# Kernel optimization log

Measured on AMD Instinct MI355X. Metric: run time of the kernel, lower is better.

## Reference

```python
import jax, jax.numpy as jnp
import numpy as np
from jax import lax

B, C, H, W = 8, 512, 48, 48
E = 512          # embed_dim (== in_channels, required by GLoR fusion channel math)
P = 128          # ContextBlock planes = int(512*0.25)
NC = 2           # num_classes; also used (buggily, but faithfully) as BGAM threshold
TOPK_RATIO = 0.1


def conv1x1(x, w, b=None):
    # w: [out, in]
    y = jnp.einsum('bchw,oc->bohw', x, w)
    if b is not None:
        y = y + b[None, :, None, None]
    return y


def conv3x3(x, w, b):
    y = lax.conv_general_dilated(x, w, (1, 1), 'SAME',
                                 dimension_numbers=('NCHW', 'OIHW', 'NCHW'))
    return y + b[None, :, None, None]


def dwconv3x3(x, w):
    # depthwise: w [C,1,3,3], feature_group_count=C
    return lax.conv_general_dilated(x, w, (1, 1), 'SAME',
                                    dimension_numbers=('NCHW', 'OIHW', 'NCHW'),
                                    feature_group_count=x.shape[1])


def bn_eval(x, g, b):
    # eval-mode BatchNorm2d, running_mean=0, running_var=1, eps=1e-5
    scale = g / jnp.sqrt(1.0 + 1e-5)
    return x * scale[None, :, None, None] + b[None, :, None, None]


def chan_mlp(c, w1, b1, g, bl, w2, b2):
    # ContextBlock channel transform: 1x1 conv -> LayerNorm([P,1,1]) -> ReLU -> 1x1 conv, on [B,C] vectors
    h = c @ w1.T + b1                                  # [B,P]
    mu = h.mean(-1, keepdims=True)
    var = jnp.var(h, axis=-1, keepdims=True)
    h = (h - mu) / jnp.sqrt(var + 1e-5) * g + bl
    h = jax.nn.relu(h)
    return h @ w2.T + b2                               # [B,C]


def cos_self(t):
    # torch F.cosine_similarity(t, t, dim=1): dot/(max(n,eps)*max(n,eps)), eps=1e-8
    nrm2 = jnp.sum(t * t, axis=1)                      # [B,H,W]
    n = jnp.maximum(jnp.sqrt(nrm2), 1e-8)
    return nrm2 / (n * n)


def setup_inputs() -> dict:
    key = jax.random.key(0)
    ks = iter(jax.random.split(key, 64))
    def nrm(shape, scale):
        return (jax.random.normal(next(ks), shape) * scale).astype(jnp.float32)
    def gma(n):
        return (1.0 + 0.05 * jax.random.normal(next(ks), (n,))).astype(jnp.float32)
    def bta(n):
        return (0.05 * jax.random.normal(next(ks), (n,))).astype(jnp.float32)
    sC = 1.0 / np.sqrt(C)
    return dict(
        x=jax.random.normal(next(ks), (B, C, H, W), jnp.float32),
        # GLoR local ConvBranch
        lb_w1=nrm((E, C), sC), lb_g1=gma(E), lb_b1=bta(E),
        lb_w2=nrm((E, 1, 3, 3), 1.0 / 3.0), lb_g2=gma(E), lb_b2=bta(E),
        lb_w3=nrm((E, E), 1.0 / np.sqrt(E)), lb_g3=gma(E), lb_b3=bta(E),
        # GLoR ContextBlock (att pooling, channel_add + channel_mul)
        cm_w=nrm((1, C), sC), cm_b=bta(1),
        ca_w1=nrm((P, C), sC), ca_b1=bta(P), ca_lg=gma(P), ca_lb=bta(P),
        ca_w2=nrm((C, P), 1.0 / np.sqrt(P)), ca_b2=bta(C),
        cmu_w1=nrm((P, C), sC), cmu_b1=bta(P), cmu_lg=gma(P), cmu_lb=bta(P),
        cmu_w2=nrm((C, P), 1.0 / np.sqrt(P)), cmu_b2=bta(C),
        fu_w=nrm((E, 2 * E), 1.0 / np.sqrt(2 * E)), fu_b=bta(E),
        # heads
        sh_w=nrm((NC, E), 1.0 / np.sqrt(E)), sh_b=bta(NC),
        bh_w=nrm((2, E), 1.0 / np.sqrt(E)), bh_b=bta(2),
        # ReverseAttention
        ra_w1=nrm((2, 2, 3, 3), 1.0 / np.sqrt(18)), ra_b1=bta(2), ra_g1=gma(2), ra_bb1=bta(2),
        ra_w2=nrm((2, 2, 3, 3), 1.0 / np.sqrt(18)), ra_b2=bta(2), ra_g2=gma(2), ra_bb2=bta(2),
        # AGCR (all bias=False)
        q_w=nrm((E // 4, E), 1.0 / np.sqrt(E)), k_w=nrm((E // 4, E), 1.0 / np.sqrt(E)),
        v_w=nrm((E, E), 1.0 / np.sqrt(E)), fin_w=nrm((E, 2 * E), 1.0 / np.sqrt(2 * E)),
    )


def reference(x, lb_w1, lb_g1, lb_b1, lb_w2, lb_g2, lb_b2, lb_w3, lb_g3, lb_b3,
              cm_w, cm_b, ca_w1, ca_b1, ca_lg, ca_lb, ca_w2, ca_b2,
              cmu_w1, cmu_b1, cmu_lg, cmu_lb, cmu_w2, cmu_b2, fu_w, fu_b,
              sh_w, sh_b, bh_w, bh_b,
              ra_w1, ra_b1, ra_g1, ra_bb1, ra_w2, ra_b2, ra_g2, ra_bb2,
              q_w, k_w, v_w, fin_w):
    b_, c_, h_, w_ = x.shape
    N = h_ * w_
    # ---- GLoR: local ConvBranch ----
    t = jax.nn.relu(bn_eval(conv1x1(x, lb_w1), lb_g1, lb_b1))
    t = jax.nn.relu(bn_eval(dwconv3x3(t, lb_w2), lb_g2, lb_b2))
    local = bn_eval(conv1x1(t, lb_w3), lb_g3, lb_b3)
    # ---- GLoR: ContextBlock (att pooling) ----
    xf = x.reshape(b_, c_, N)
    mask = (conv1x1(x, cm_w, cm_b)).reshape(b_, 1, N)
    mask = jax.nn.softmax(mask, axis=2)
    ctx = jnp.einsum('bcn,bn->bc', xf, mask[:, 0, :])              # [B,C]
    mul = jax.nn.sigmoid(chan_mlp(ctx, cmu_w1, cmu_b1, cmu_lg, cmu_lb, cmu_w2, cmu_b2))
    add = chan_mlp(ctx, ca_w1, ca_b1, ca_lg, ca_lb, ca_w2, ca_b2)
    glob = x * mul[:, :, None, None] + add[:, :, None, None]
    gx = conv1x1(jnp.concatenate([local, glob], axis=1), fu_w, fu_b)  # [B,E,H,W]
    # ---- heads ----
    sem = conv1x1(gx, sh_w, sh_b)                                   # [B,NC,H,W]
    bdl = conv1x1(gx, bh_w, bh_b)                                   # [B,2,H,W]
    # ---- ReverseAttention(boundary_logits, sigmoid(boundary_logits)) ----
    wx = bdl * (1.0 - jax.nn.sigmoid(bdl))
    r = jax.nn.relu(bn_eval(conv3x3(wx, ra_w1, ra_b1), ra_g1, ra_bb1))
    r = jax.nn.relu(bn_eval(conv3x3(r, ra_w2, ra_b2), ra_g2, ra_bb2))
    # ---- BGAM (threshold = num_classes, faithful to source) ----
    thr = jnp.float32(NC)
    st = (cos_self(sem) > thr).astype(x.dtype)
    bt = (cos_self(r) > thr).astype(x.dtype)
    region = ((1.0 - st) * (1.0 - bt))[:, None]                     # [B,1,H,W]
    # ---- AGCR custom attention ----
    k_num = int(N * TOPK_RATIO)
    q = conv1x1(gx, q_w).reshape(b_, -1, N)                         # [B,E/4,N]
    kk = conv1x1(gx, k_w).reshape(b_, -1, N)
    v = conv1x1(gx, v_w).reshape(b_, E, N)
    attn = jnp.einsum('bdm,bdn->bmn', q, kk) / jnp.sqrt(jnp.float32(q.shape[1]))
    aw = jax.nn.softmax(attn, axis=-1)                              # [B,N,N]
    topv, _ = lax.top_k(aw, k_num)
    soft = topv.mean(-1)                                            # [B,N]
    aw = aw * soft[:, None, :]
    # bmm(value, aw^T).mean(-1) == value @ aw.mean(rows)
    col_mean = aw.mean(axis=1)                                      # [B,N]
    ctx2 = jnp.einsum('bcn,bn->bc', v, col_mean)                    # [B,E]
    ctx2 = jnp.broadcast_to(ctx2[:, :, None, None], gx.shape)
    refined = jnp.concatenate([gx, ctx2 * region], axis=1)          # [B,2E,H,W]
    return conv1x1(refined, fin_w)                                  # [B,E,H,W]
```

## Files before the change

### kernel.cpp

```cpp
#include <hip/hip_runtime.h>
#include <math.h>

#define NPIX 2304
#define NCH  512
#define NB   8
#define KNUM 230

typedef unsigned short u16;
typedef __attribute__((ext_vector_type(8))) short short8v;
typedef __attribute__((ext_vector_type(4))) float float4v;

__device__ __forceinline__ float bf2f(u16 u) {
    union { unsigned v; float f; } x; x.v = ((unsigned)u) << 16; return x.f;
}
__device__ __forceinline__ u16 f2bf(float f) {
    union { float f; unsigned v; } x; x.f = f;
    unsigned r = x.v + 0x7FFFu + ((x.v >> 16) & 1u);
    return (u16)(r >> 16);
}

__device__ __forceinline__ float waveSum(float v) {
    #pragma unroll
    for (int o = 32; o > 0; o >>= 1) v += __shfl_down(v, o);
    return v;
}
__device__ __forceinline__ float blockSum256(float v, float* sc4) {
    v = waveSum(v);
    __syncthreads();
    if ((threadIdx.x & 63) == 0) sc4[threadIdx.x >> 6] = v;
    __syncthreads();
    return sc4[0] + sc4[1] + sc4[2] + sc4[3];
}
__device__ __forceinline__ float waveMaxF(float v) {
    #pragma unroll
    for (int o = 32; o > 0; o >>= 1) v = fmaxf(v, __shfl_down(v, o));
    return v;
}
__device__ __forceinline__ float blockMax256(float v, float* sc4) {
    v = waveMaxF(v);
    __syncthreads();
    if ((threadIdx.x & 63) == 0) sc4[threadIdx.x >> 6] = v;
    __syncthreads();
    return fmaxf(fmaxf(sc4[0], sc4[1]), fmaxf(sc4[2], sc4[3]));
}

__device__ __forceinline__ void gl_lds16(const u16* g, u16* l) {
    __builtin_amdgcn_global_load_lds(
        reinterpret_cast<const unsigned __attribute__((address_space(1)))*>(
            reinterpret_cast<uintptr_t>(g)),
        reinterpret_cast<unsigned __attribute__((address_space(3)))*>(
            reinterpret_cast<uintptr_t>(l)),
        16, 0, 0);
}

__global__ __launch_bounds__(256, 2) void mfma_gemm(
    const u16* __restrict__ A, int ldA, long sA,
    const u16* __restrict__ B0, const u16* __restrict__ B1, int ldB, long sB,
    void* __restrict__ outp, int ldO, long sO,
    const float* __restrict__ scaleR, const float* __restrict__ biasR,
    const float* __restrict__ biasC, int ldbc,
    int K, float alpha, int flags)
{
    __shared__ u16 lA[128 * 64];
    __shared__ u16 lB[128 * 64];
    const int t  = threadIdx.x;
    const int w  = t >> 6, l = t & 63;
    const int wR = w >> 1, wC = w & 1;
    const int lg = l >> 4, lr = l & 15, l7 = l & 7;
    const int b   = blockIdx.z;
    const int Cl0 = blockIdx.x * 128;
    const int R0  = blockIdx.y * 128;
    const u16* Ab  = A + (size_t)b * sA;
    const u16* B0b = B0 + (size_t)b * sB;
    const u16* B1b = B1 ? B1 + (size_t)b * sB : nullptr;

    float4v acc[4][4];
    const float4v zero = {0.f, 0.f, 0.f, 0.f};
    #pragma unroll
    for (int i = 0; i < 4; ++i)
        #pragma unroll
        for (int j = 0; j < 4; ++j) acc[i][j] = zero;

    const int sr = t >> 3;
    const int sp = t & 7;

    for (int k0 = 0; k0 < K; k0 += 64) {
        const u16* Bsrc = B0b; int kb = k0;
        if (B1b && k0 >= 512) { Bsrc = B1b; kb = k0 - 512; }
        #pragma unroll
        for (int i = 0; i < 4; ++i) {
            const int r  = i * 32 + sr;
            const int ca = sp ^ (r & 7);
            gl_lds16(Ab   + (size_t)(R0  + r) * ldA + (k0 + ca * 8), &lA[i * 2048 + t * 8]);
            gl_lds16(Bsrc + (size_t)(Cl0 + r) * ldB + (kb + ca * 8), &lB[i * 2048 + t * 8]);
        }
        __syncthreads();
        #pragma unroll
        for (int kk = 0; kk < 2; ++kk) {
            short8v af[4], bfv[4];
            const int p = (kk * 4 + lg) ^ l7;
            #pragma unroll
            for (int mt = 0; mt < 4; ++mt) {
                const int rA = wR * 64 + mt * 16 + lr;
                af[mt]  = *reinterpret_cast<const short8v*>(&lA[rA * 64 + p * 8]);
                const int rB = wC * 64 + mt * 16 + lr;
                bfv[mt] = *reinterpret_cast<const short8v*>(&lB[rB * 64 + p * 8]);
            }
            #pragma unroll
            for (int mt = 0; mt < 4; ++mt)
                #pragma unroll
                for (int nt = 0; nt < 4; ++nt)
                    acc[mt][nt] = __builtin_amdgcn_mfma_f32_16x16x32_bf16(
                        af[mt], bfv[nt], acc[mt][nt], 0, 0, 0);
        }
        __syncthreads();
    }

    const bool relu = (flags & 1), f32o = (flags & 2);
    #pragma unroll
    for (int nt = 0; nt < 4; ++nt) {
        const int Cl = Cl0 + wC * 64 + nt * 16 + lr;
        const float bc = biasC ? biasC[(size_t)b * ldbc + Cl] : 0.f;
        #pragma unroll
        for (int mt = 0; mt < 4; ++mt) {
            const int Rb = R0 + wR * 64 + mt * 16 + lg * 4;
            float4 scv = scaleR ? *reinterpret_cast<const float4*>(&scaleR[Rb])
                                : make_float4(1.f, 1.f, 1.f, 1.f);
            float4 bv  = biasR  ? *reinterpret_cast<const float4*>(&biasR[Rb])
                                : make_float4(0.f, 0.f, 0.f, 0.f);
            float vals[4];
            #pragma unroll
            for (int j = 0; j < 4; ++j) {
                const float sc = alpha * ((&scv.x)[j]);
                float v = acc[mt][nt][j] * sc + (&bv.x)[j] + bc;
                if (relu) v = fmaxf(v, 0.f);
                vals[j] = v;
            }
            if (f32o) {
                float* op = (float*)outp + (size_t)b * sO + (size_t)Cl * ldO + Rb;
                *reinterpret_cast<float4*>(op) = make_float4(vals[0], vals[1], vals[2], vals[3]);
            } else {
                ushort4 u;
                u.x = f2bf(vals[0]); u.y = f2bf(vals[1]);
                u.z = f2bf(vals[2]); u.w = f2bf(vals[3]);
                u16* op = (u16*)outp + (size_t)b * sO + (size_t)Cl * ldO + Rb;
                *reinterpret_cast<ushort4*>(op) = u;
            }
        }
    }
}

__global__ __launch_bounds__(256) void transpose_cvt(
    const float* __restrict__ x, u16* __restrict__ xb)
{
    __shared__ float tile[64][65];
    const int t = threadIdx.x;
    const int n0 = blockIdx.x * 64, c0 = blockIdx.y * 64, b = blockIdx.z;
    const int tr = t >> 4, tc4 = (t & 15) * 4;
    #pragma unroll
    for (int i = 0; i < 4; ++i) {
        const int cc = tr + i * 16;
        float4 v = *reinterpret_cast<const float4*>(
            x + ((size_t)(b * NCH + c0 + cc)) * NPIX + n0 + tc4);
        tile[cc][tc4 + 0] = v.x; tile[cc][tc4 + 1] = v.y;
        tile[cc][tc4 + 2] = v.z; tile[cc][tc4 + 3] = v.w;
    }
    __syncthreads();
    #pragma unroll
    for (int i = 0; i < 4; ++i) {
        const int nn = tr + i * 16;
        ushort4 u;
        u.x = f2bf(tile[tc4 + 0][nn]); u.y = f2bf(tile[tc4 + 1][nn]);
        u.z = f2bf(tile[tc4 + 2][nn]); u.w = f2bf(tile[tc4 + 3][nn]);
        *reinterpret_cast<ushort4*>(xb + ((size_t)b * NPIX + n0 + nn) * NCH + c0 + tc4) = u;
    }
}

__global__ __launch_bounds__(256) void cvt_bf16(
    const float* __restrict__ s, u16* __restrict__ d, int n4)
{
    const int i = blockIdx.x * 256 + threadIdx.x;
    if (i < n4) {
        float4 v = reinterpret_cast<const float4*>(s)[i];
        ushort4 u; u.x = f2bf(v.x); u.y = f2bf(v.y); u.z = f2bf(v.z); u.w = f2bf(v.w);
        reinterpret_cast<ushort4*>(d)[i] = u;
    }
}

__global__ __launch_bounds__(256) void fold_dw(
    const float* __restrict__ wsrc, const float* __restrict__ g, float* __restrict__ wf)
{
    const int i = blockIdx.x * 256 + threadIdx.x;
    if (i < 9 * NCH) {
        const int c = i / 9, tap = i % 9;
        wf[tap * NCH + c] = wsrc[i] * g[c] * 0.99999500003749978f;
    }
}

__global__ __launch_bounds__(256) void dwconv_k(
    const u16* __restrict__ t1, const float* __restrict__ wf,
    const float* __restrict__ b2, u16* __restrict__ t2)
{
    const int idx = blockIdx.x * 256 + threadIdx.x;
    const int cq = idx & 127;
    const int n  = (idx >> 7) % NPIX;
    const int b  = (idx >> 7) / NPIX;
    const int c  = cq * 4;
    const int y = n / 48, x = n % 48;
    float s0 = 0.f, s1 = 0.f, s2 = 0.f, s3 = 0.f;
    #pragma unroll
    for (int dy = -1; dy <= 1; ++dy) {
        const int yy = y + dy;
        if (yy < 0 || yy >= 48) continue;
        #pragma unroll
        for (int dx = -1; dx <= 1; ++dx) {
            const int xx = x + dx;
            if (xx < 0 || xx >= 48) continue;
            ushort4 tv = *reinterpret_cast<const ushort4*>(
                &t1[((size_t)b * NPIX + yy * 48 + xx) * NCH + c]);
            float4 wv = *reinterpret_cast<const float4*>(
                &wf[((dy + 1) * 3 + dx + 1) * NCH + c]);
            s0 = fmaf(bf2f(tv.x), wv.x, s0); s1 = fmaf(bf2f(tv.y), wv.y, s1);
            s2 = fmaf(bf2f(tv.z), wv.z, s2); s3 = fmaf(bf2f(tv.w), wv.w, s3);
        }
    }
    float4 bb = *reinterpret_cast<const float4*>(&b2[c]);
    ushort4 o;
    o.x = f2bf(fmaxf(s0 + bb.x, 0.f)); o.y = f2bf(fmaxf(s1 + bb.y, 0.f));
    o.z = f2bf(fmaxf(s2 + bb.z, 0.f)); o.w = f2bf(fmaxf(s3 + bb.w, 0.f));
    *reinterpret_cast<ushort4*>(&t2[((size_t)b * NPIX + n) * NCH + c]) = o;
}

__global__ __launch_bounds__(256) void mask_logits_k(
    const u16* __restrict__ xb, const float* __restrict__ cmw,
    const float* __restrict__ cmb, float* __restrict__ logits)
{
    const int w = threadIdx.x >> 6, l = threadIdx.x & 63;
    const int n = blockIdx.x * 4 + w, b = blockIdx.y;
    const ushort4* row = reinterpret_cast<const ushort4*>(xb + ((size_t)b * NPIX + n) * NCH);
    const int c0 = l * 8;
    ushort4 u0 = row[l * 2], u1 = row[l * 2 + 1];
    float4 w0 = *reinterpret_cast<const float4*>(&cmw[c0]);
    float4 w1 = *reinterpret_cast<const float4*>(&cmw[c0 + 4]);
    float s = bf2f(u0.x) * w0.x + bf2f(u0.y) * w0.y + bf2f(u0.z) * w0.z + bf2f(u0.w) * w0.w
            + bf2f(u1.x) * w1.x + bf2f(u1.y) * w1.y + bf2f(u1.z) * w1.z + bf2f(u1.w) * w1.w;
    s = waveSum(s);
    if (l == 0) logits[(size_t)b * NPIX + n] = s + cmb[0];
}

__global__ __launch_bounds__(256) void softmax_mask(
    const float* __restrict__ logits, float* __restrict__ mask)
{
    __shared__ float sc[4];
    const int b = blockIdx.x, t = threadIdx.x;
    const float* lr = logits + (size_t)b * NPIX;
    float mx = -3.4e38f;
    for (int i = t; i < NPIX; i += 256) mx = fmaxf(mx, lr[i]);
    mx = blockMax256(mx, sc);
    float s = 0.f;
    for (int i = t; i < NPIX; i += 256) s += __expf(lr[i] - mx);
    s = blockSum256(s, sc);
    const float inv = 1.0f / s;
    for (int i = t; i < NPIX; i += 256) mask[(size_t)b * NPIX + i] = __expf(lr[i] - mx) * inv;
}

__global__ __launch_bounds__(512) void ctx_pool_k(
    const u16* __restrict__ xb, const float* __restrict__ mask, float* __restrict__ ctx)
{
    const int c = threadIdx.x, b = blockIdx.y;
    const int nn0 = blockIdx.x * 128;
    float s = 0.f;
    for (int n = nn0; n < nn0 + 128; ++n)
        s = fmaf(bf2f(xb[((size_t)b * NPIX + n) * NCH + c]), mask[(size_t)b * NPIX + n], s);
    atomicAdd(&ctx[b * NCH + c], s);
}

__global__ __launch_bounds__(256) void chan_mlp2(
    const float* __restrict__ ctxv,
    const float* __restrict__ mw1, const float* __restrict__ mb1,
    const float* __restrict__ mlg, const float* __restrict__ mlb,
    const float* __restrict__ mw2, const float* __restrict__ mb2,
    const float* __restrict__ aw1, const float* __restrict__ ab1,
    const float* __restrict__ alg, const float* __restrict__ alb,
    const float* __restrict__ aw2, const float* __restrict__ ab2,
    float* __restrict__ mulo, float* __restrict__ addo)
{
    __shared__ float cs[512];
    __shared__ float hn[128];
    __shared__ float sc4[4];
    const int path = blockIdx.x, b = blockIdx.y;
    const int t = threadIdx.x, w = t >> 6, l = t & 63;
    const float* W1 = path ? aw1 : mw1;
    const float* B1 = path ? ab1 : mb1;
    const float* LG = path ? alg : mlg;
    const float* LB = path ? alb : mlb;
    const float* W2 = path ? aw2 : mw2;
    const float* B2 = path ? ab2 : mb2;
    cs[t]       = ctxv[b * 512 + t];
    cs[t + 256] = ctxv[b * 512 + 256 + t];
    __syncthreads();
    const float4 ca = *reinterpret_cast<const float4*>(&cs[l * 8]);
    const float4 cb = *reinterpret_cast<const float4*>(&cs[l * 8 + 4]);
    #pragma unroll 4
    for (int hh = 0; hh < 32; ++hh) {
        const int h = w * 32 + hh;
        const float4 wa = *reinterpret_cast<const float4*>(&W1[h * 512 + l * 8]);
        const float4 wb = *reinterpret_cast<const float4*>(&W1[h * 512 + l * 8 + 4]);
        float s = wa.x * ca.x + wa.y * ca.y + wa.z * ca.z + wa.w * ca.w
                + wb.x * cb.x + wb.y * cb.y + wb.z * cb.z + wb.w * cb.w;
        s = waveSum(s);
        if (l == 0) hn[h] = s + B1[h];
    }
    __syncthreads();
    const float v = (t < 128) ? hn[t] : 0.f;
    const float s1 = blockSum256(v, sc4);
    const float mu = s1 * (1.0f / 128.0f);
    const float d = (t < 128) ? (v - mu) : 0.f;
    const float s2 = blockSum256(d * d, sc4);
    const float var = s2 * (1.0f / 128.0f);
    if (t < 128) hn[t] = fmaxf(d / sqrtf(var + 1e-5f) * LG[t] + LB[t], 0.f);
    __syncthreads();
    #pragma unroll
    for (int oo = 0; oo < 2; ++oo) {
        const int o = t + oo * 256;
        float s = B2[o];
        #pragma unroll
        for (int p = 0; p < 128; p += 4) {
            const float4 wv = *reinterpret_cast<const float4*>(&W2[o * 128 + p]);
            s += wv.x * hn[p] + wv.y * hn[p + 1] + wv.z * hn[p + 2] + wv.w * hn[p + 3];
        }
        if (path == 0) mulo[b * 512 + o] = 1.0f / (1.0f + __expf(-s));
        else           addo[b * 512 + o] = s;
    }
}

__global__ __launch_bounds__(256) void glob_ew_k(
    const u16* __restrict__ xb, const float* __restrict__ mulv,
    const float* __restrict__ addv, u16* __restrict__ g)
{
    const int idx = blockIdx.x * 256 + threadIdx.x;
    const int cq = idx & 63;
    const int n = (idx >> 6) % NPIX;
    const int b = (idx >> 6) / NPIX;
    const int c = cq * 8;
    const size_t base = ((size_t)b * NPIX + n) * NCH + c;
    ushort4 u0 = *reinterpret_cast<const ushort4*>(&xb[base]);
    ushort4 u1 = *reinterpret_cast<const ushort4*>(&xb[base + 4]);
    const float* mp = &mulv[b * NCH + c];
    const float* ap = &addv[b * NCH + c];
    float4 m0 = *reinterpret_cast<const float4*>(mp);
    float4 m1 = *reinterpret_cast<const float4*>(mp + 4);
    float4 a0 = *reinterpret_cast<const float4*>(ap);
    float4 a1 = *reinterpret_cast<const float4*>(ap + 4);
    ushort4 o0, o1;
    o0.x = f2bf(fmaf(bf2f(u0.x), m0.x, a0.x));
    o0.y = f2bf(fmaf(bf2f(u0.y), m0.y, a0.y));
    o0.z = f2bf(fmaf(bf2f(u0.z), m0.z, a0.z));
    o0.w = f2bf(fmaf(bf2f(u0.w), m0.w, a0.w));
    o1.x = f2bf(fmaf(bf2f(u1.x), m1.x, a1.x));
    o1.y = f2bf(fmaf(bf2f(u1.y), m1.y, a1.y));
    o1.z = f2bf(fmaf(bf2f(u1.z), m1.z, a1.z));
    o1.w = f2bf(fmaf(bf2f(u1.w), m1.w, a1.w));
    *reinterpret_cast<ushort4*>(&g[base]) = o0;
    *reinterpret_cast<ushort4*>(&g[base + 4]) = o1;
}

__global__ __launch_bounds__(256) void softmax_topk_wave(
    const u16* __restrict__ p, float* __restrict__ mxo,
    float* __restrict__ invSo, float* __restrict__ softo, int bOff)
{
    const int w = threadIdx.x >> 6, l = threadIdx.x & 63;
    const int r = blockIdx.x * 4 + w;
    const int bc = blockIdx.y;
    const u16* pr = p + ((size_t)bc * NPIX + r) * NPIX;
    const uint4* p16 = reinterpret_cast<const uint4*>(pr);
    uint4 q0 = p16[l], q1 = p16[64 + l], q2 = p16[128 + l], q3 = p16[192 + l];
    uint2 q4 = reinterpret_cast<const uint2*>(pr)[512 + l];
    unsigned uw[18] = {q0.x, q0.y, q0.z, q0.w, q1.x, q1.y, q1.z, q1.w,
                       q2.x, q2.y, q2.z, q2.w, q3.x, q3.y, q3.z, q3.w,
                       q4.x, q4.y};
    unsigned km[36];
    #pragma unroll
    for (int i = 0; i < 18; ++i) {
        const unsigned v = uw[i];
        const unsigned m = ((v >> 15) & 0x10001u) * 0x7FFFu + 0x80008000u;
        const unsigned s = v ^ m;
        km[2 * i]     = s & 0xFFFFu;
        km[2 * i + 1] = s >> 16;
    }
    unsigned kmax = km[0];
    #pragma unroll
    for (int i = 1; i < 36; ++i) kmax = max(kmax, km[i]);
    #pragma unroll
    for (int o = 32; o > 0; o >>= 1) kmax = max(kmax, (unsigned)__shfl_xor((int)kmax, o));
    const unsigned mxbits = (kmax & 0x8000u) ? (kmax ^ 0x8000u) : (kmax ^ 0xFFFFu);
    const float mx = bf2f((u16)mxbits);
    unsigned kt = 0u;
    for (int bit = 15; bit >= 0; --bit) {
        const unsigned cand = kt | (1u << bit);
        int c = 0;
        #pragma unroll
        for (int i = 0; i < 36; ++i)
            c += (int)__popcll(__ballot(km[i] >= cand));
        if (c >= KNUM) kt = cand;
    }
    const unsigned tbits = (kt & 0x8000u) ? (kt ^ 0x8000u) : (kt ^ 0xFFFFu);
    const float te = __expf(bf2f((u16)tbits) - mx);
    float S = 0.f, ss = 0.f; int a = 0;
    #pragma unroll
    for (int i = 0; i < 36; ++i) {
        const unsigned bb = (km[i] & 0x8000u) ? (km[i] ^ 0x8000u) : (km[i] ^ 0xFFFFu);
        const float e = __expf(bf2f((u16)bb) - mx);
        S += e;
        const bool gt = km[i] > kt;
        if (gt) ss += e;
        a += (int)__popcll(__ballot(gt));
    }
    #pragma unroll
    for (int o = 32; o > 0; o >>= 1) { S += __shfl_xor(S, o); ss += __shfl_xor(ss, o); }
    if (l == 0) {
        const size_t gi = (size_t)(bOff + bc) * NPIX + r;
        mxo[gi] = mx; invSo[gi] = 1.0f / S;
        softo[gi] = (ss + (float)(KNUM - a) * te) / (S * (float)KNUM);
    }
}

__global__ __launch_bounds__(256) void colsum_k(
    const u16* __restrict__ p, const float* __restrict__ mxo,
    const float* __restrict__ invSo, float* __restrict__ colsum, int bOff)
{
    const int j = blockIdx.x * 256 + threadIdx.x;
    const int ic0 = blockIdx.y * 72;
    const int bc = blockIdx.z;
    const float* mxr = mxo + (size_t)(bOff + bc) * NPIX;
    const float* isr = invSo + (size_t)(bOff + bc) * NPIX;
    const u16* pb = p + (size_t)bc * NPIX * NPIX;
    float s = 0.f;
    #pragma unroll 4
    for (int i = ic0; i < ic0 + 72; ++i)
        s += __expf(bf2f(pb[(size_t)i * NPIX + j]) - mxr[i]) * isr[i];
    atomicAdd(&colsum[(size_t)(bOff + bc) * NPIX + j], s);
}

__global__ __launch_bounds__(512) void ctx2_pool_k(
    const u16* __restrict__ qkv, const float* __restrict__ colsum,
    const float* __restrict__ soft, float* __restrict__ ctx2)
{
    const int c = threadIdx.x, b = blockIdx.y;
    const int nn0 = blockIdx.x * 128;
    float s = 0.f;
    for (int n = nn0; n < nn0 + 128; ++n) {
        const float wgt = colsum[(size_t)b * NPIX + n] * soft[(size_t)b * NPIX + n];
        s = fmaf(bf2f(qkv[((size_t)b * NPIX + n) * 768 + 256 + c]), wgt, s);
    }
    atomicAdd(&ctx2[b * NCH + c], s * (1.0f / (float)NPIX));
}

__global__ __launch_bounds__(256) void compute_z(
    const float* __restrict__ finw, const float* __restrict__ ctx2, float* __restrict__ z)
{
    const int o = blockIdx.x * 256 + threadIdx.x;
    const int b = blockIdx.y;
    const float* c2 = ctx2 + b * NCH;
    const float* wr = finw + (size_t)o * 1024 + 512;
    float s = 0.f;
    for (int c = 0; c < NCH; ++c) s = fmaf(wr[c], c2[c], s);
    z[b * NCH + o] = s;
}

extern "C" void kernel_launch(void* const* d_in, const int* in_sizes, int n_in,
                              void* d_out, int out_size, void* d_ws, size_t ws_size,
                              hipStream_t stream)
{
    (void)in_sizes; (void)n_in; (void)out_size; (void)ws_size;
    const float* x      = (const float*)d_in[0];
    const float* lb_w1  = (const float*)d_in[1];
    const float* lb_g1  = (const float*)d_in[2];
    const float* lb_b1  = (const float*)d_in[3];
    const float* lb_w2  = (const float*)d_in[4];
    const float* lb_g2  = (const float*)d_in[5];
    const float* lb_b2  = (const float*)d_in[6];
    const float* lb_w3  = (const float*)d_in[7];
    const float* lb_g3  = (const float*)d_in[8];
    const float* lb_b3  = (const float*)d_in[9];
    const float* cm_w   = (const float*)d_in[10];
    const float* cm_b   = (const float*)d_in[11];
    const float* ca_w1  = (const float*)d_in[12];
    const float* ca_b1  = (const float*)d_in[13];
    const float* ca_lg  = (const float*)d_in[14];
    const float* ca_lb  = (const float*)d_in[15];
    const float* ca_w2  = (const float*)d_in[16];
    const float* ca_b2  = (const float*)d_in[17];
    const float* cmu_w1 = (const float*)d_in[18];
    const float* cmu_b1 = (const float*)d_in[19];
    const float* cmu_lg = (const float*)d_in[20];
    const float* cmu_lb = (const float*)d_in[21];
    const float* cmu_w2 = (const float*)d_in[22];
    const float* cmu_b2 = (const float*)d_in[23];
    const float* fu_w   = (const float*)d_in[24];
    const float* fu_b   = (const float*)d_in[25];
    const float* q_w    = (const float*)d_in[38];
    const float* k_w    = (const float*)d_in[39];
    const float* v_w    = (const float*)d_in[40];
    const float* fin_w  = (const float*)d_in[41];

    char* W = (char*)d_ws;
    const size_t SZ_ACT = (size_t)NB * NPIX * NCH * 2;
    u16* xb   = (u16*)(W);
    u16* bufA = (u16*)(W + SZ_ACT);
    u16* bufB = (u16*)(W + 2 * SZ_ACT);
    u16* gx   = (u16*)(W + 3 * SZ_ACT);
    u16* qkv  = (u16*)(W + 4 * SZ_ACT);
    char* SM = W + 4 * SZ_ACT + (size_t)NB * NPIX * 768 * 2;
    float* logits = (float*)SM; SM += (size_t)NB * NPIX * 4;
    float* maskb  = (float*)SM; SM += (size_t)NB * NPIX * 4;
    float* mxb    = (float*)SM; SM += (size_t)NB * NPIX * 4;
    float* invSb  = (float*)SM; SM += (size_t)NB * NPIX * 4;
    float* softb  = (float*)SM; SM += (size_t)NB * NPIX * 4;
    float* colsum = (float*)SM; SM += (size_t)NB * NPIX * 4;
    float* ctxb   = (float*)SM; SM += (size_t)NB * NCH * 4;
    float* ctx2b  = (float*)SM; SM += (size_t)NB * NCH * 4;
    float* mulb   = (float*)SM; SM += (size_t)NB * NCH * 4;
    float* addb   = (float*)SM; SM += (size_t)NB * NCH * 4;
    float* zbuf   = (float*)SM; SM += (size_t)NB * NCH * 4;
    float* wfold  = (float*)SM; SM += (size_t)9 * NCH * 4;
    u16* w1b   = (u16*)SM; SM += (size_t)512 * 512 * 2;
    u16* w3b   = (u16*)SM; SM += (size_t)512 * 512 * 2;
    u16* fuwb  = (u16*)SM; SM += (size_t)512 * 1024 * 2;
    u16* finwb = (u16*)SM; SM += (size_t)512 * 1024 * 2;
    u16* qkvwb = (u16*)SM; SM += (size_t)768 * 512 * 2;
    u16* pbuf = xb;

    const float invs  = 0.99999500003749978f;
    const float rs128 = 0.08838834764831845f;
    const long SACT = (long)NPIX * NCH;

    cvt_bf16<<<256, 256, 0, stream>>>(lb_w1, w1b, 65536);
    cvt_bf16<<<256, 256, 0, stream>>>(lb_w3, w3b, 65536);
    cvt_bf16<<<512, 256, 0, stream>>>(fu_w, fuwb, 131072);
    cvt_bf16<<<512, 256, 0, stream>>>(fin_w, finwb, 131072);
    cvt_bf16<<<64, 256, 0, stream>>>(q_w, qkvwb, 16384);
    cvt_bf16<<<64, 256, 0, stream>>>(k_w, qkvwb + 128 * 512, 16384);
    cvt_bf16<<<256, 256, 0, stream>>>(v_w, qkvwb + 256 * 512, 65536);
    fold_dw<<<18, 256, 0, stream>>>(lb_w2, lb_g2, wfold);
    transpose_cvt<<<dim3(36, 8, 8), 256, 0, stream>>>(x, xb);
    hipMemsetAsync(colsum, 0, (size_t)NB * NPIX * 4 + 2 * (size_t)NB * NCH * 4, stream);

    mfma_gemm<<<dim3(18, 4, 8), 256, 0, stream>>>(w1b, 512, 0, xb, nullptr, 512, SACT,
        bufA, 512, SACT, lb_g1, lb_b1, nullptr, 0, 512, invs, 1);
    dwconv_k<<<9216, 256, 0, stream>>>(bufA, wfold, lb_b2, bufB);
    mfma_gemm<<<dim3(18, 4, 8), 256, 0, stream>>>(w3b, 512, 0, bufB, nullptr, 512, SACT,
        bufA, 512, SACT, lb_g3, lb_b3, nullptr, 0, 512, invs, 0);
    mask_logits_k<<<dim3(576, 8), 256, 0, stream>>>(xb, cm_w, cm_b, logits);
    softmax_mask<<<8, 256, 0, stream>>>(logits, maskb);
    ctx_pool_k<<<dim3(18, 8), 512, 0, stream>>>(xb, maskb, ctxb);
    chan_mlp2<<<dim3(2, 8), 256, 0, stream>>>(ctxb,
        cmu_w1, cmu_b1, cmu_lg, cmu_lb, cmu_w2, cmu_b2,
        ca_w1, ca_b1, ca_lg, ca_lb, ca_w2, ca_b2, mulb, addb);
    glob_ew_k<<<4608, 256, 0, stream>>>(xb, mulb, addb, bufB);
    mfma_gemm<<<dim3(18, 4, 8), 256, 0, stream>>>(fuwb, 1024, 0, bufA, bufB, 512, SACT,
        gx, 512, SACT, nullptr, fu_b, nullptr, 0, 1024, 1.0f, 0);
    mfma_gemm<<<dim3(18, 6, 8), 256, 0, stream>>>(qkvwb, 512, 0, gx, nullptr, 512, SACT,
        qkv, 768, (long)NPIX * 768, nullptr, nullptr, nullptr, 0, 512, 1.0f, 0);
    for (int cc = 0; cc < 2; ++cc) {
        const u16* kp = qkv + (size_t)cc * 4 * NPIX * 768 + 128;
        const u16* qp = qkv + (size_t)cc * 4 * NPIX * 768;
        mfma_gemm<<<dim3(18, 18, 4), 256, 0, stream>>>(kp, 768, (long)NPIX * 768,
            qp, nullptr, 768, (long)NPIX * 768,
            pbuf, NPIX, (long)NPIX * NPIX, nullptr, nullptr, nullptr, 0, 128, rs128, 0);
        softmax_topk_wave<<<dim3(576, 4), 256, 0, stream>>>(pbuf, mxb, invSb, softb, cc * 4);
        colsum_k<<<dim3(9, 32, 4), 256, 0, stream>>>(pbuf, mxb, invSb, colsum, cc * 4);
    }
    ctx2_pool_k<<<dim3(18, 8), 512, 0, stream>>>(qkv, colsum, softb, ctx2b);
    compute_z<<<dim3(2, 8), 256, 0, stream>>>(fin_w, ctx2b, zbuf);
    mfma_gemm<<<dim3(4, 18, 8), 256, 0, stream>>>(gx, 512, SACT, finwb, nullptr, 1024, 0,
        d_out, NPIX, (long)NCH * NPIX, nullptr, nullptr, zbuf, 512, 512, 1.0f, 2);
}
```

Measured before the change: 402.7 us.

## Split channel MLP into three wide kernels and raise GEMM occupancy hint

The single 16-block channel-MLP kernel is replaced by three kernels: a first-layer matvec spread across 2048 waves, a LayerNorm+ReLU kernel, and a second-layer kernel with 64 blocks. The goal is to expose more parallelism on what was a latency-bound, low-occupancy step. It costs two extra launches and a small global round-trip through a new buffer. Separately, the GEMM launch bounds go from 2 to 3 blocks per CU, which may limit registers and cause spills.

```diff
diff --git a/kernel.cpp b/kernel.cpp
--- a/kernel.cpp
+++ b/kernel.cpp
@@ -53,7 +53,7 @@
         16, 0, 0);
 }
 
-__global__ __launch_bounds__(256, 2) void mfma_gemm(
+__global__ __launch_bounds__(256, 3) void mfma_gemm(
     const u16* __restrict__ A, int ldA, long sA,
     const u16* __restrict__ B0, const u16* __restrict__ B1, int ldB, long sB,
     void* __restrict__ outp, int ldO, long sO,
@@ -275,63 +275,74 @@
     atomicAdd(&ctx[b * NCH + c], s);
 }
 
-__global__ __launch_bounds__(256) void chan_mlp2(
+__global__ __launch_bounds__(256) void chan_h(
     const float* __restrict__ ctxv,
     const float* __restrict__ mw1, const float* __restrict__ mb1,
+    const float* __restrict__ aw1, const float* __restrict__ ab1,
+    float* __restrict__ hnb)
+{
+    const int w = threadIdx.x >> 6, l = threadIdx.x & 63;
+    const int gid = blockIdx.x * 4 + w;
+    const int path = gid >> 10;
+    const int rem  = gid & 1023;
+    const int h = rem >> 3, b = rem & 7;
+    const float* W1 = path ? aw1 : mw1;
+    const float* B1 = path ? ab1 : mb1;
+    const float4 wa = *reinterpret_cast<const float4*>(&W1[h * 512 + l * 8]);
+    const float4 wb = *reinterpret_cast<const float4*>(&W1[h * 512 + l * 8 + 4]);
+    const float4 ca = *reinterpret_cast<const float4*>(&ctxv[b * 512 + l * 8]);
+    const float4 cb = *reinterpret_cast<const float4*>(&ctxv[b * 512 + l * 8 + 4]);
+    float s = wa.x * ca.x + wa.y * ca.y + wa.z * ca.z + wa.w * ca.w
+            + wb.x * cb.x + wb.y * cb.y + wb.z * cb.z + wb.w * cb.w;
+    s = waveSum(s);
+    if (l == 0) hnb[(path * 8 + b) * 128 + h] = s + B1[h];
+}
+
+__global__ __launch_bounds__(128) void chan_ln(
     const float* __restrict__ mlg, const float* __restrict__ mlb,
+    const float* __restrict__ alg, const float* __restrict__ alb,
+    float* __restrict__ hnb)
+{
+    __shared__ float sc[2];
+    const int path = blockIdx.x, b = blockIdx.y, t = threadIdx.x;
+    float* hp = hnb + (path * 8 + b) * 128;
+    const float v = hp[t];
+    float s1 = waveSum(v);
+    if ((t & 63) == 0) sc[t >> 6] = s1;
+    __syncthreads();
+    const float mu = (sc[0] + sc[1]) * (1.0f / 128.0f);
+    const float d = v - mu;
+    float s2 = waveSum(d * d);
+    __syncthreads();
+    if ((t & 63) == 0) sc[t >> 6] = s2;
+    __syncthreads();
+    const float var = (sc[0] + sc[1]) * (1.0f / 128.0f);
+    const float* LG = path ? alg : mlg;
+    const float* LB = path ? alb : mlb;
+    hp[t] = fmaxf(d / sqrtf(var + 1e-5f) * LG[t] + LB[t], 0.f);
+}
+
+__global__ __launch_bounds__(128) void chan_o(
+    const float* __restrict__ hnb,
     const float* __restrict__ mw2, const float* __restrict__ mb2,
-    const float* __restrict__ aw1, const float* __restrict__ ab1,
-    const float* __restrict__ alg, const float* __restrict__ alb,
     const float* __restrict__ aw2, const float* __restrict__ ab2,
     float* __restrict__ mulo, float* __restrict__ addo)
 {
-    __shared__ float cs[512];
-    __shared__ float hn[128];
-    __shared__ float sc4[4];
-    const int path = blockIdx.x, b = blockIdx.y;
-    const int t = threadIdx.x, w = t >> 6, l = t & 63;
-    const float* W1 = path ? aw1 : mw1;
-    const float* B1 = path ? ab1 : mb1;
-    const float* LG = path ? alg : mlg;
-    const float* LB = path ? alb : mlb;
+    __shared__ float hs[128];
+    const int oc = blockIdx.x, path = blockIdx.y, b = blockIdx.z;
+    const int t = threadIdx.x;
+    hs[t] = hnb[(path * 8 + b) * 128 + t];
+    __syncthreads();
+    const int o = oc * 128 + t;
     const float* W2 = path ? aw2 : mw2;
-    const float* B2 = path ? ab2 : mb2;
-    cs[t]       = ctxv[b * 512 + t];
-    cs[t + 256] = ctxv[b * 512 + 256 + t];
-    __syncthreads();
-    const float4 ca = *reinterpret_cast<const float4*>(&cs[l * 8]);
-    const float4 cb = *reinterpret_cast<const float4*>(&cs[l * 8 + 4]);
-    #pragma unroll 4
-    for (int hh = 0; hh < 32; ++hh) {
-        const int h = w * 32 + hh;
-        const float4 wa = *reinterpret_cast<const float4*>(&W1[h * 512 + l * 8]);
-        const float4 wb = *reinterpret_cast<const float4*>(&W1[h * 512 + l * 8 + 4]);
-        float s = wa.x * ca.x + wa.y * ca.y + wa.z * ca.z + wa.w * ca.w
-                + wb.x * cb.x + wb.y * cb.y + wb.z * cb.z + wb.w * cb.w;
-        s = waveSum(s);
-        if (l == 0) hn[h] = s + B1[h];
-    }
-    __syncthreads();
-    const float v = (t < 128) ? hn[t] : 0.f;
-    const float s1 = blockSum256(v, sc4);
-    const float mu = s1 * (1.0f / 128.0f);
-    const float d = (t < 128) ? (v - mu) : 0.f;
-    const float s2 = blockSum256(d * d, sc4);
-    const float var = s2 * (1.0f / 128.0f);
-    if (t < 128) hn[t] = fmaxf(d / sqrtf(var + 1e-5f) * LG[t] + LB[t], 0.f);
-    __syncthreads();
-    #pragma unroll
-    for (int oo = 0; oo < 2; ++oo) {
-        const int o = t + oo * 256;
-        float s = B2[o];
-        #pragma unroll
-        for (int p = 0; p < 128; p += 4) {
-            const float4 wv = *reinterpret_cast<const float4*>(&W2[o * 128 + p]);
-            s += wv.x * hn[p] + wv.y * hn[p + 1] + wv.z * hn[p + 2] + wv.w * hn[p + 3];
-        }
-        if (path == 0) mulo[b * 512 + o] = 1.0f / (1.0f + __expf(-s));
-        else           addo[b * 512 + o] = s;
-    }
+    float s = (path ? ab2 : mb2)[o];
+    #pragma unroll
+    for (int p = 0; p < 128; p += 4) {
+        const float4 wv = *reinterpret_cast<const float4*>(&W2[o * 128 + p]);
+        s += wv.x * hs[p] + wv.y * hs[p + 1] + wv.z * hs[p + 2] + wv.w * hs[p + 3];
+    }
+    if (path == 0) mulo[b * 512 + o] = 1.0f / (1.0f + __expf(-s));
+    else           addo[b * 512 + o] = s;
 }
 
 __global__ __launch_bounds__(256) void glob_ew_k(
@@ -523,6 +534,7 @@
     float* mulb   = (float*)SM; SM += (size_t)NB * NCH * 4;
     float* addb   = (float*)SM; SM += (size_t)NB * NCH * 4;
     float* zbuf   = (float*)SM; SM += (size_t)NB * NCH * 4;
+    float* hnb    = (float*)SM; SM += (size_t)2 * NB * 128 * 4;
     float* wfold  = (float*)SM; SM += (size_t)9 * NCH * 4;
     u16* w1b   = (u16*)SM; SM += (size_t)512 * 512 * 2;
     u16* w3b   = (u16*)SM; SM += (size_t)512 * 512 * 2;
@@ -554,9 +566,9 @@
     mask_logits_k<<<dim3(576, 8), 256, 0, stream>>>(xb, cm_w, cm_b, logits);
     softmax_mask<<<8, 256, 0, stream>>>(logits, maskb);
     ctx_pool_k<<<dim3(18, 8), 512, 0, stream>>>(xb, maskb, ctxb);
-    chan_mlp2<<<dim3(2, 8), 256, 0, stream>>>(ctxb,
-        cmu_w1, cmu_b1, cmu_lg, cmu_lb, cmu_w2, cmu_b2,
-        ca_w1, ca_b1, ca_lg, ca_lb, ca_w2, ca_b2, mulb, addb);
+    chan_h<<<512, 256, 0, stream>>>(ctxb, cmu_w1, cmu_b1, ca_w1, ca_b1, hnb);
+    chan_ln<<<dim3(2, 8), 128, 0, stream>>>(cmu_lg, cmu_lb, ca_lg, ca_lb, hnb);
+    chan_o<<<dim3(4, 2, 8), 128, 0, stream>>>(hnb, cmu_w2, cmu_b2, ca_w2, ca_b2, mulb, addb);
     glob_ew_k<<<4608, 256, 0, stream>>>(xb, mulb, addb, bufB);
     mfma_gemm<<<dim3(18, 4, 8), 256, 0, stream>>>(fuwb, 1024, 0, bufA, bufB, 512, SACT,
         gx, 512, SACT, nullptr, fu_b, nullptr, 0, 1024, 1.0f, 0);
```

After: 382.1 us. -5.1%, faster.
